# Optimization experiments

Measured on AMD Instinct MI355X. Metric: run time of the kernel, lower is better.

The kernel has to match this reference:

```python
import math
import jax, jax.numpy as jnp
import numpy as np

N, K, D = 500_000, 16, 8
TWO_PI = 2.0 * math.pi


def setup_inputs() -> dict:
    key = jax.random.key(0)
    k0, k1, k2, k3 = jax.random.split(key, 4)
    X = jax.random.normal(k0, (N, D), jnp.float32)
    mu = jax.random.normal(k1, (K, D), jnp.float32)
    L = jax.random.normal(k2, (K, D, D), jnp.float32) * 0.3
    # positive weights keep the (squared-weight) mixture pdf strictly positive
    weights = jax.random.uniform(k3, (K,), jnp.float32, 0.2, 1.0)
    return {"X": X, "mu": mu, "L": L, "weights": weights, "it": 0}


def reference(X, mu, L, weights, it):
    # Covariances via Cholesky composition: tril(L) @ tril(L)^T + I   [K,D,D]
    Lt = jnp.tril(L)
    sig = Lt @ jnp.swapaxes(Lt, -1, -2) + jnp.eye(D, dtype=X.dtype)
    prec = jnp.linalg.inv(sig)                     # sigma_k^{-1}      [K,D,D]

    # Pairwise squared params: P_ij = prec_i + prec_j, Sigma_ij = P_ij^{-1}
    P = prec[:, None] + prec[None, :]              # [K,K,D,D]
    Sig_pair = jnp.linalg.inv(P)                   # [K,K,D,D]
    rhs = jnp.einsum('kde,ke->kd', prec, mu)       # prec_k @ mu_k     [K,D]
    rp = rhs[:, None, :] + rhs[None, :, :]         # [K,K,D]
    mu_pair = jnp.einsum('ijde,ije->ijd', Sig_pair, rp)  # [K,K,D]

    # z_ij = 1/sqrt(det((2*pi)^D * Sigma_ij))  (faithful: scalar scales the matrix
    # before det, giving (2*pi)^(D*D) * det(Sigma))
    detS = jnp.linalg.det(Sig_pair)                # [K,K]
    z = 1.0 / jnp.sqrt((TWO_PI ** D) ** D * detS)  # [K,K]

    Pf = P.reshape(K * K, D * D)                   # [K^2, D^2]
    Xo = (X[:, :, None] * X[:, None, :]).reshape(-1, D * D)  # [N, D^2]
    xPx = Xo @ Pf.T                                # [N, K^2]
    b = jnp.einsum('ijde,ije->ijd', P, mu_pair).reshape(K * K, D)  # P mu  [K^2,D]
    xPmu = X @ b.T                                 # [N, K^2]
    muPmu = jnp.einsum('pd,pd->p', mu_pair.reshape(K * K, D), b)   # [K^2]
    quad = xPx - 2.0 * xPmu + muPmu[None, :]       # [N, K^2]

    wpair = (weights[:, None] * weights[None, :]).reshape(-1)      # [K^2]
    pdf = jnp.exp(-0.5 * quad) @ (z.reshape(-1) * wpair)           # [N]

    # Faithful quirk: original returns z * pdf where z is from the LAST (i,j)
    # pair, i.e. (K-1, K-1).
    z_last = z.reshape(-1)[-1]
    return jnp.log(z_last * pdf).mean()
```

## Files before the change

### kernel.cpp

```cpp
#include <hip/hip_runtime.h>
#include <math.h>


#define LOG2E_F 1.4426950408889634f
#define LN2_F   0.6931471805599453f
#define LN2PI_F 1.8378770664093453f

#define WS_COEF 0
#define WS_ES   768
#define WS_K    1024
#define WS_PART 1088

typedef float f2 __attribute__((ext_vector_type(2)));

__device__ const int EOFF_D[16] = {0,4,8,12,16,24,32,40,48,60,72,84,96,112,128,144};

__device__ __forceinline__ float fexp2(float x) {
#if __has_builtin(__builtin_amdgcn_exp2f)
  return __builtin_amdgcn_exp2f(x);
#else
  return exp2f(x);
#endif
}
__device__ __forceinline__ float flog2(float x) {
#if __has_builtin(__builtin_amdgcn_logf)
  return __builtin_amdgcn_logf(x);
#else
  return log2f(x);
#endif
}
__device__ __forceinline__ f2 vfma(float c, f2 x, f2 a) {
  return __builtin_elementwise_fma((f2){c, c}, x, a);
}

__device__ __forceinline__ void chol8(const float (*A)[8], float (*C)[8]) {
  #pragma unroll
  for (int d = 0; d < 8; ++d) {
    float s = A[d][d];
    #pragma unroll
    for (int m = 0; m < 8; ++m) if (m < d) s -= C[d][m] * C[d][m];
    float cd = sqrtf(s);
    C[d][d] = cd;
    float inv = 1.f / cd;
    #pragma unroll
    for (int e = 0; e < 8; ++e) if (e > d) {
      float t = A[e][d];
      #pragma unroll
      for (int m = 0; m < 8; ++m) if (m < d) t -= C[e][m] * C[d][m];
      C[e][d] = t * inv;
    }
  }
}

__global__ __launch_bounds__(256) void gm_setup(const float* __restrict__ mu,
                                                const float* __restrict__ L,
                                                const float* __restrict__ wts,
                                                float* __restrict__ ws) {
  __shared__ float sp[16][72];
  int tid = threadIdx.x;
  ws[768 + tid] = 0.f;
  if (tid < 16) {
    int k = tid;
    float Lt[8][8];
    #pragma unroll
    for (int d = 0; d < 8; ++d)
      #pragma unroll
      for (int e = 0; e < 8; ++e)
        Lt[d][e] = (e <= d) ? L[k * 64 + d * 8 + e] : 0.f;
    float A[8][8];
    #pragma unroll
    for (int d = 0; d < 8; ++d)
      #pragma unroll
      for (int e = 0; e <= d; ++e) {
        float s = (d == e) ? 1.f : 0.f;
        #pragma unroll
        for (int m = 0; m < 8; ++m) s += Lt[d][m] * Lt[e][m];
        A[d][e] = s;
        A[e][d] = s;
      }
    float C[8][8];
    chol8(A, C);
    float Ci[8][8];
    #pragma unroll
    for (int d = 0; d < 8; ++d) Ci[d][d] = 1.f / C[d][d];
    #pragma unroll
    for (int e = 0; e < 8; ++e)
      #pragma unroll
      for (int d = 0; d < 8; ++d) if (d > e) {
        float s = 0.f;
        #pragma unroll
        for (int m = 0; m < 8; ++m) if (m >= e && m < d) s += C[d][m] * Ci[m][e];
        Ci[d][e] = -s * Ci[d][d];
      }
    #pragma unroll
    for (int a = 0; a < 8; ++a)
      #pragma unroll
      for (int b = 0; b < 8; ++b) {
        float s = 0.f;
        #pragma unroll
        for (int m = 0; m < 8; ++m) if (m >= a && m >= b) s += Ci[m][a] * Ci[m][b];
        sp[k][a * 8 + b] = s;
      }
    #pragma unroll
    for (int d = 0; d < 8; ++d) {
      float s = 0.f;
      #pragma unroll
      for (int e = 0; e < 8; ++e) s += sp[k][d * 8 + e] * mu[k * 8 + e];
      sp[k][64 + d] = s;
    }
  }
  __syncthreads();

  int p = tid;
  int i = p >> 4, j = p & 15;
  const float* pi = sp[i];
  const float* pj = sp[j];
  float P[8][8], rp[8];
  #pragma unroll
  for (int d = 0; d < 8; ++d) {
    #pragma unroll
    for (int e = 0; e < 8; ++e) P[d][e] = pi[d * 8 + e] + pj[d * 8 + e];
    rp[d] = pi[64 + d] + pj[64 + d];
  }
  float U[8][8];
  chol8(P, U);
  float logdet = 0.f;
  #pragma unroll
  for (int d = 0; d < 8; ++d) logdet += logf(U[d][d]);
  logdet *= 2.f;
  float zf[8];
  #pragma unroll
  for (int d = 0; d < 8; ++d) {
    float s = rp[d];
    #pragma unroll
    for (int m = 0; m < 8; ++m) if (m < d) s -= U[d][m] * zf[m];
    zf[d] = s / U[d][d];
  }
  float y[8];
  #pragma unroll
  for (int dd = 7; dd >= 0; --dd) {
    float s = zf[dd];
    #pragma unroll
    for (int m = 0; m < 8; ++m) if (m > dd) s -= U[m][dd] * y[m];
    y[dd] = s / U[dd][dd];
  }
  float muPmu = 0.f;
  #pragma unroll
  for (int d = 0; d < 8; ++d) muPmu += rp[d] * y[d];
  float c = -0.5f * muPmu + 0.5f * logdet - 32.f * LN2PI_F
          + logf(wts[i]) + logf(wts[j]) + 64.f * LN2_F;
  float Ev = expf(c);
  if (j <= i)
    ws[WS_ES + EOFF_D[i] + j] = (i == j) ? Ev : 2.f * Ev;
  if (i == j) {
    float* c0 = ws + WS_COEF + i * 48;
    int q = 0;
    #pragma unroll
    for (int d = 0; d < 8; ++d) {
      c0[q++] = pi[64 + d] * LOG2E_F;
      #pragma unroll
      for (int e = d; e < 8; ++e) {
        float v = (d == e) ? -0.5f * pi[d * 8 + e] : -pi[d * 8 + e];
        c0[q++] = v * LOG2E_F;
      }
    }
    c0[44] = 0.f; c0[45] = 0.f; c0[46] = 0.f; c0[47] = 0.f;
  }
  if (p == 255) ws[WS_K] = 0.5f * logdet - 32.f * LN2PI_F - 64.f * LN2_F;
}

__global__ __launch_bounds__(256) void gm_main(const float* __restrict__ X,
                                               const float* __restrict__ cf,
                                               float* __restrict__ partials,
                                               int N) {
  __shared__ float sc[1024];
  {
    const float4* cf4 = reinterpret_cast<const float4*>(cf);
    reinterpret_cast<float4*>(sc)[threadIdx.x] = cf4[threadIdx.x];
  }

  const int t = threadIdx.x;
  const int base = blockIdx.x * 1024 + t;
  bool act[4];
  float4 xa[4], xb[4];
  #pragma unroll
  for (int g = 0; g < 4; ++g) {
    int gid = base + g * 256;
    act[g] = gid < N;
    const float4* Xv =
        reinterpret_cast<const float4*>(X) + (size_t)(act[g] ? gid : 0) * 2;
    xa[g] = Xv[0];
    xb[g] = Xv[1];
  }
  __syncthreads();

  f2 xs01[8], xs23[8];
  xs01[0] = (f2){xa[0].x, xa[1].x}; xs23[0] = (f2){xa[2].x, xa[3].x};
  xs01[1] = (f2){xa[0].y, xa[1].y}; xs23[1] = (f2){xa[2].y, xa[3].y};
  xs01[2] = (f2){xa[0].z, xa[1].z}; xs23[2] = (f2){xa[2].z, xa[3].z};
  xs01[3] = (f2){xa[0].w, xa[1].w}; xs23[3] = (f2){xa[2].w, xa[3].w};
  xs01[4] = (f2){xb[0].x, xb[1].x}; xs23[4] = (f2){xb[2].x, xb[3].x};
  xs01[5] = (f2){xb[0].y, xb[1].y}; xs23[5] = (f2){xb[2].y, xb[3].y};
  xs01[6] = (f2){xb[0].z, xb[1].z}; xs23[6] = (f2){xb[2].z, xb[3].z};
  xs01[7] = (f2){xb[0].w, xb[1].w}; xs23[7] = (f2){xb[2].w, xb[3].w};

  constexpr int D_OF[44] = {0,0,0,0,0,0,0,0,0,
                            1,1,1,1,1,1,1,1,
                            2,2,2,2,2,2,2,
                            3,3,3,3,3,3,
                            4,4,4,4,4,
                            5,5,5,5,
                            6,6,6,
                            7,7};
  constexpr int E_OF[44] = {-1,0,1,2,3,4,5,6,7,
                            -1,1,2,3,4,5,6,7,
                            -1,2,3,4,5,6,7,
                            -1,3,4,5,6,7,
                            -1,4,5,6,7,
                            -1,5,6,7,
                            -1,6,7,
                            -1,7};

  f2 u01[16], u23[16];
  #pragma unroll
  for (int i = 0; i < 16; ++i) {
    const float4* c4 = reinterpret_cast<const float4*>(sc + i * 48);
    f2 g01 = (f2){0.f, 0.f}, g23 = (f2){0.f, 0.f};
    f2 r01 = (f2){0.f, 0.f}, r23 = (f2){0.f, 0.f};
    #pragma unroll
    for (int v = 0; v < 11; ++v) {
      float4 w = c4[v];
      #pragma unroll
      for (int k2 = 0; k2 < 4; ++k2) {
        const int q = 4 * v + k2;
        const float cc = (k2 == 0) ? w.x : (k2 == 1) ? w.y : (k2 == 2) ? w.z : w.w;
        if (E_OF[q] < 0) {
          if (q > 0) {
            g01 = __builtin_elementwise_fma(xs01[D_OF[q - 1]], r01, g01);
            g23 = __builtin_elementwise_fma(xs23[D_OF[q - 1]], r23, g23);
          }
          r01 = (f2){cc, cc};
          r23 = (f2){cc, cc};
        } else {
          r01 = vfma(cc, xs01[E_OF[q]], r01);
          r23 = vfma(cc, xs23[E_OF[q]], r23);
        }
      }
    }
    g01 = __builtin_elementwise_fma(xs01[7], r01, g01);
    g23 = __builtin_elementwise_fma(xs23[7], r23, g23);
    u01[i] = (f2){fexp2(g01.x), fexp2(g01.y)};
    u23[i] = (f2){fexp2(g23.x), fexp2(g23.y)};
  }

  constexpr int EOFF[16]  = {0,4,8,12,16,24,32,40,48,60,72,84,96,112,128,144};
  constexpr int ELEN4[16] = {1,1,1,1,2,2,2,2,3,3,3,3,4,4,4,4};
  const float4* es4 = reinterpret_cast<const float4*>(sc + 768);
  f2 pdf01 = (f2){0.f, 0.f}, pdf23 = (f2){0.f, 0.f};
  #pragma unroll
  for (int i = 0; i < 16; ++i) {
    f2 s01 = (f2){0.f, 0.f}, s23 = (f2){0.f, 0.f};
    #pragma unroll
    for (int q4 = 0; q4 < ELEN4[i]; ++q4) {
      float4 ev = es4[EOFF[i] / 4 + q4];
      const int j = q4 * 4;
      s01 = vfma(ev.x, u01[j + 0], s01); s23 = vfma(ev.x, u23[j + 0], s23);
      s01 = vfma(ev.y, u01[j + 1], s01); s23 = vfma(ev.y, u23[j + 1], s23);
      s01 = vfma(ev.z, u01[j + 2], s01); s23 = vfma(ev.z, u23[j + 2], s23);
      s01 = vfma(ev.w, u01[j + 3], s01); s23 = vfma(ev.w, u23[j + 3], s23);
    }
    pdf01 = __builtin_elementwise_fma(u01[i], s01, pdf01);
    pdf23 = __builtin_elementwise_fma(u23[i], s23, pdf23);
  }
  float lsum = 0.f;
  if (act[0]) lsum += flog2(pdf01.x);
  if (act[1]) lsum += flog2(pdf01.y);
  if (act[2]) lsum += flog2(pdf23.x);
  if (act[3]) lsum += flog2(pdf23.y);

  #pragma unroll
  for (int off = 32; off > 0; off >>= 1) lsum += __shfl_down(lsum, off, 64);
  __shared__ float wsum[4];
  int lane = threadIdx.x & 63, wid = threadIdx.x >> 6;
  if (lane == 0) wsum[wid] = lsum;
  __syncthreads();
  if (threadIdx.x == 0)
    partials[blockIdx.x] = (wsum[0] + wsum[1]) + (wsum[2] + wsum[3]);
}

__global__ __launch_bounds__(256) void gm_final(const float* __restrict__ ws,
                                                float* __restrict__ out,
                                                int nb, float invN) {
  const float* partials = ws + WS_PART;
  float s = 0.f;
  for (int t = threadIdx.x; t < nb; t += 256) s += partials[t];
  #pragma unroll
  for (int off = 32; off > 0; off >>= 1) s += __shfl_down(s, off, 64);
  __shared__ float wsum[4];
  int lane = threadIdx.x & 63, wid = threadIdx.x >> 6;
  if (lane == 0) wsum[wid] = s;
  __syncthreads();
  if (threadIdx.x == 0) {
    float tot = (wsum[0] + wsum[1]) + (wsum[2] + wsum[3]);
    out[0] = tot * LN2_F * invN + ws[WS_K];
  }
}

extern "C" void kernel_launch(void* const* d_in, const int* in_sizes, int n_in,
                              void* d_out, int out_size, void* d_ws, size_t ws_size,
                              hipStream_t stream) {
  const float* X = (const float*)d_in[0];
  const float* mu = (const float*)d_in[1];
  const float* L = (const float*)d_in[2];
  const float* wts = (const float*)d_in[3];
  float* ws = (float*)d_ws;
  float* out = (float*)d_out;
  int N = in_sizes[0] / 8;
  int nb = (N + 1023) / 1024;
  gm_setup<<<1, 256, 0, stream>>>(mu, L, wts, ws);
  gm_main<<<nb, 256, 0, stream>>>(X, ws, ws + WS_PART, N);
  gm_final<<<1, 256, 0, stream>>>(ws, out, nb, 1.0f / (float)N);
}
```

Measured before the change: 24.25 us.

## Fuse parameter setup into main kernel, recomputing coefficients per block

Removes the single-block setup kernel and has every block of the main kernel redo the covariance Cholesky, pairwise factorisations and coefficient generation straight into shared memory, issuing its X loads first so they overlap that work. This removes one kernel launch and the serial dependency on a one-block kernel, and avoids a global round trip of the coefficients. The cost is redundant setup math in each of roughly 489 blocks (16 serial 8x8 factorisations plus 256 pair Cholesky solves per block) and higher register pressure, with launch bounds raised to request two blocks per CU.

```diff
diff --git a/kernel.cpp b/kernel.cpp
--- a/kernel.cpp
+++ b/kernel.cpp
@@ -6,8 +6,6 @@
 #define LN2_F   0.6931471805599453f
 #define LN2PI_F 1.8378770664093453f
 
-#define WS_COEF 0
-#define WS_ES   768
 #define WS_K    1024
 #define WS_PART 1088
 
@@ -52,135 +50,17 @@
   }
 }
 
-__global__ __launch_bounds__(256) void gm_setup(const float* __restrict__ mu,
-                                                const float* __restrict__ L,
-                                                const float* __restrict__ wts,
-                                                float* __restrict__ ws) {
+__global__ __launch_bounds__(256, 2) void gm_all(const float* __restrict__ X,
+                                                 const float* __restrict__ mu,
+                                                 const float* __restrict__ L,
+                                                 const float* __restrict__ wts,
+                                                 float* __restrict__ ws,
+                                                 int N) {
   __shared__ float sp[16][72];
-  int tid = threadIdx.x;
-  ws[768 + tid] = 0.f;
-  if (tid < 16) {
-    int k = tid;
-    float Lt[8][8];
-    #pragma unroll
-    for (int d = 0; d < 8; ++d)
-      #pragma unroll
-      for (int e = 0; e < 8; ++e)
-        Lt[d][e] = (e <= d) ? L[k * 64 + d * 8 + e] : 0.f;
-    float A[8][8];
-    #pragma unroll
-    for (int d = 0; d < 8; ++d)
-      #pragma unroll
-      for (int e = 0; e <= d; ++e) {
-        float s = (d == e) ? 1.f : 0.f;
-        #pragma unroll
-        for (int m = 0; m < 8; ++m) s += Lt[d][m] * Lt[e][m];
-        A[d][e] = s;
-        A[e][d] = s;
-      }
-    float C[8][8];
-    chol8(A, C);
-    float Ci[8][8];
-    #pragma unroll
-    for (int d = 0; d < 8; ++d) Ci[d][d] = 1.f / C[d][d];
-    #pragma unroll
-    for (int e = 0; e < 8; ++e)
-      #pragma unroll
-      for (int d = 0; d < 8; ++d) if (d > e) {
-        float s = 0.f;
-        #pragma unroll
-        for (int m = 0; m < 8; ++m) if (m >= e && m < d) s += C[d][m] * Ci[m][e];
-        Ci[d][e] = -s * Ci[d][d];
-      }
-    #pragma unroll
-    for (int a = 0; a < 8; ++a)
-      #pragma unroll
-      for (int b = 0; b < 8; ++b) {
-        float s = 0.f;
-        #pragma unroll
-        for (int m = 0; m < 8; ++m) if (m >= a && m >= b) s += Ci[m][a] * Ci[m][b];
-        sp[k][a * 8 + b] = s;
-      }
-    #pragma unroll
-    for (int d = 0; d < 8; ++d) {
-      float s = 0.f;
-      #pragma unroll
-      for (int e = 0; e < 8; ++e) s += sp[k][d * 8 + e] * mu[k * 8 + e];
-      sp[k][64 + d] = s;
-    }
-  }
-  __syncthreads();
-
-  int p = tid;
-  int i = p >> 4, j = p & 15;
-  const float* pi = sp[i];
-  const float* pj = sp[j];
-  float P[8][8], rp[8];
-  #pragma unroll
-  for (int d = 0; d < 8; ++d) {
-    #pragma unroll
-    for (int e = 0; e < 8; ++e) P[d][e] = pi[d * 8 + e] + pj[d * 8 + e];
-    rp[d] = pi[64 + d] + pj[64 + d];
-  }
-  float U[8][8];
-  chol8(P, U);
-  float logdet = 0.f;
-  #pragma unroll
-  for (int d = 0; d < 8; ++d) logdet += logf(U[d][d]);
-  logdet *= 2.f;
-  float zf[8];
-  #pragma unroll
-  for (int d = 0; d < 8; ++d) {
-    float s = rp[d];
-    #pragma unroll
-    for (int m = 0; m < 8; ++m) if (m < d) s -= U[d][m] * zf[m];
-    zf[d] = s / U[d][d];
-  }
-  float y[8];
-  #pragma unroll
-  for (int dd = 7; dd >= 0; --dd) {
-    float s = zf[dd];
-    #pragma unroll
-    for (int m = 0; m < 8; ++m) if (m > dd) s -= U[m][dd] * y[m];
-    y[dd] = s / U[dd][dd];
-  }
-  float muPmu = 0.f;
-  #pragma unroll
-  for (int d = 0; d < 8; ++d) muPmu += rp[d] * y[d];
-  float c = -0.5f * muPmu + 0.5f * logdet - 32.f * LN2PI_F
-          + logf(wts[i]) + logf(wts[j]) + 64.f * LN2_F;
-  float Ev = expf(c);
-  if (j <= i)
-    ws[WS_ES + EOFF_D[i] + j] = (i == j) ? Ev : 2.f * Ev;
-  if (i == j) {
-    float* c0 = ws + WS_COEF + i * 48;
-    int q = 0;
-    #pragma unroll
-    for (int d = 0; d < 8; ++d) {
-      c0[q++] = pi[64 + d] * LOG2E_F;
-      #pragma unroll
-      for (int e = d; e < 8; ++e) {
-        float v = (d == e) ? -0.5f * pi[d * 8 + e] : -pi[d * 8 + e];
-        c0[q++] = v * LOG2E_F;
-      }
-    }
-    c0[44] = 0.f; c0[45] = 0.f; c0[46] = 0.f; c0[47] = 0.f;
-  }
-  if (p == 255) ws[WS_K] = 0.5f * logdet - 32.f * LN2PI_F - 64.f * LN2_F;
-}
-
-__global__ __launch_bounds__(256) void gm_main(const float* __restrict__ X,
-                                               const float* __restrict__ cf,
-                                               float* __restrict__ partials,
-                                               int N) {
   __shared__ float sc[1024];
-  {
-    const float4* cf4 = reinterpret_cast<const float4*>(cf);
-    reinterpret_cast<float4*>(sc)[threadIdx.x] = cf4[threadIdx.x];
-  }
-
-  const int t = threadIdx.x;
-  const int base = blockIdx.x * 1024 + t;
+  const int tid = threadIdx.x;
+
+  const int base = blockIdx.x * 1024 + tid;
   bool act[4];
   float4 xa[4], xb[4];
   #pragma unroll
@@ -191,6 +71,120 @@
         reinterpret_cast<const float4*>(X) + (size_t)(act[g] ? gid : 0) * 2;
     xa[g] = Xv[0];
     xb[g] = Xv[1];
+  }
+
+  sc[768 + tid] = 0.f;
+
+  if (tid < 16) {
+    int k = tid;
+    float Lt[8][8];
+    #pragma unroll
+    for (int d = 0; d < 8; ++d)
+      #pragma unroll
+      for (int e = 0; e < 8; ++e)
+        Lt[d][e] = (e <= d) ? L[k * 64 + d * 8 + e] : 0.f;
+    float A[8][8];
+    #pragma unroll
+    for (int d = 0; d < 8; ++d)
+      #pragma unroll
+      for (int e = 0; e <= d; ++e) {
+        float s = (d == e) ? 1.f : 0.f;
+        #pragma unroll
+        for (int m = 0; m < 8; ++m) s += Lt[d][m] * Lt[e][m];
+        A[d][e] = s;
+        A[e][d] = s;
+      }
+    float C[8][8];
+    chol8(A, C);
+    float Ci[8][8];
+    #pragma unroll
+    for (int d = 0; d < 8; ++d) Ci[d][d] = 1.f / C[d][d];
+    #pragma unroll
+    for (int e = 0; e < 8; ++e)
+      #pragma unroll
+      for (int d = 0; d < 8; ++d) if (d > e) {
+        float s = 0.f;
+        #pragma unroll
+        for (int m = 0; m < 8; ++m) if (m >= e && m < d) s += C[d][m] * Ci[m][e];
+        Ci[d][e] = -s * Ci[d][d];
+      }
+    #pragma unroll
+    for (int a = 0; a < 8; ++a)
+      #pragma unroll
+      for (int b = 0; b < 8; ++b) {
+        float s = 0.f;
+        #pragma unroll
+        for (int m = 0; m < 8; ++m) if (m >= a && m >= b) s += Ci[m][a] * Ci[m][b];
+        sp[k][a * 8 + b] = s;
+      }
+    #pragma unroll
+    for (int d = 0; d < 8; ++d) {
+      float s = 0.f;
+      #pragma unroll
+      for (int e = 0; e < 8; ++e) s += sp[k][d * 8 + e] * mu[k * 8 + e];
+      sp[k][64 + d] = s;
+    }
+  }
+  __syncthreads();
+
+  {
+    const int p = tid;
+    const int i = p >> 4, j = p & 15;
+    const float* pi = sp[i];
+    const float* pj = sp[j];
+    float P[8][8], rp[8];
+    #pragma unroll
+    for (int d = 0; d < 8; ++d) {
+      #pragma unroll
+      for (int e = 0; e < 8; ++e) P[d][e] = pi[d * 8 + e] + pj[d * 8 + e];
+      rp[d] = pi[64 + d] + pj[64 + d];
+    }
+    float U[8][8];
+    chol8(P, U);
+    float logdet = 0.f;
+    #pragma unroll
+    for (int d = 0; d < 8; ++d) logdet += logf(U[d][d]);
+    logdet *= 2.f;
+    float zf[8];
+    #pragma unroll
+    for (int d = 0; d < 8; ++d) {
+      float s = rp[d];
+      #pragma unroll
+      for (int m = 0; m < 8; ++m) if (m < d) s -= U[d][m] * zf[m];
+      zf[d] = s / U[d][d];
+    }
+    float y[8];
+    #pragma unroll
+    for (int dd = 7; dd >= 0; --dd) {
+      float s = zf[dd];
+      #pragma unroll
+      for (int m = 0; m < 8; ++m) if (m > dd) s -= U[m][dd] * y[m];
+      y[dd] = s / U[dd][dd];
+    }
+    float muPmu = 0.f;
+    #pragma unroll
+    for (int d = 0; d < 8; ++d) muPmu += rp[d] * y[d];
+    float c = -0.5f * muPmu + 0.5f * logdet - 32.f * LN2PI_F
+            + logf(wts[i]) + logf(wts[j]) + 64.f * LN2_F;
+    float Ev = expf(c);
+    if (j <= i)
+      sc[768 + EOFF_D[i] + j] = (i == j) ? Ev : 2.f * Ev;
+    if (i == j) {
+      float* c0 = sc + i * 48;
+      int q = 0;
+      #pragma unroll
+      for (int d = 0; d < 8; ++d) {
+        c0[q++] = pi[64 + d] * LOG2E_F;
+        #pragma unroll
+        for (int e = d; e < 8; ++e) {
+          float v = (d == e) ? -0.5f * pi[d * 8 + e] : -pi[d * 8 + e];
+          c0[q++] = v * LOG2E_F;
+        }
+      }
+      c0[44] = 0.f; c0[45] = 0.f; c0[46] = 0.f; c0[47] = 0.f;
+    }
+    if (blockIdx.x == 0 && p == 255)
+      ws[WS_K] = 0.5f * logdet - 32.f * LN2PI_F - 64.f * LN2_F;
   }
   __syncthreads();
 
@@ -285,7 +279,7 @@
   if (lane == 0) wsum[wid] = lsum;
   __syncthreads();
   if (threadIdx.x == 0)
-    partials[blockIdx.x] = (wsum[0] + wsum[1]) + (wsum[2] + wsum[3]);
+    ws[WS_PART + blockIdx.x] = (wsum[0] + wsum[1]) + (wsum[2] + wsum[3]);
 }
 
 __global__ __launch_bounds__(256) void gm_final(const float* __restrict__ ws,
@@ -317,7 +311,6 @@
   float* out = (float*)d_out;
   int N = in_sizes[0] / 8;
   int nb = (N + 1023) / 1024;
-  gm_setup<<<1, 256, 0, stream>>>(mu, L, wts, ws);
-  gm_main<<<nb, 256, 0, stream>>>(X, ws, ws + WS_PART, N);
+  gm_all<<<nb, 256, 0, stream>>>(X, mu, L, wts, ws, N);
   gm_final<<<1, 256, 0, stream>>>(ws, out, nb, 1.0f / (float)N);
 }
```

Measured after the change: 25.29 us. 4.3% more time.
